# Kernel optimization log

Hardware: AMD Instinct MI355X
Metric: run time of the kernel (lower is better)

## Reference

```python
import jax, jax.numpy as jnp
import numpy as np

B, NQ, NK = 32, 1, 4096
Q_SIZE = K_SIZE = 512
H = 256


def setup_inputs() -> dict:
    key = jax.random.key(0)
    ks = jax.random.split(key, 6)
    return {
        "queries": jax.random.normal(ks[0], (B, NQ, Q_SIZE), jnp.float32),
        "keys": jax.random.normal(ks[1], (B, NK, K_SIZE), jnp.float32),
        "values": jax.random.normal(ks[2], (B, NK, 1), jnp.float32),
        "W_q": jax.random.normal(ks[3], (Q_SIZE, H), jnp.float32) / np.sqrt(Q_SIZE),
        "W_k": jax.random.normal(ks[4], (K_SIZE, H), jnp.float32) / np.sqrt(K_SIZE),
        "w_v": jax.random.normal(ks[5], (H,), jnp.float32) / np.sqrt(H),
    }


def reference(queries, keys, values, W_q, W_k, w_v):
    # Project queries and keys to hidden dim
    q = jnp.einsum("bqd,dh->bqh", queries, W_q)            # [B, NQ, H]
    k = jnp.einsum("bkd,dh->bkh", keys, W_k)               # [B, NK, H]
    # Broadcast-add + tanh: [B, NQ, NK, H]
    features = jnp.tanh(q[:, :, None, :] + k[:, None, :, :])
    # Reduce hidden dim with w_v -> scores [B, NQ, NK]
    scores = jnp.einsum("bqkh,h->bqk", features, w_v)
    attn = jax.nn.softmax(scores, axis=-1)                 # [B, NQ, NK]
    # Module squeezes n_q dim (==1) and trailing value dim (==1)
    return attn[:, 0, :] * values[:, :, 0]                 # [B, NK]
```

## Files before the change

kernel.cpp:

```cpp
#include <hip/hip_runtime.h>
#include <cstdint>
#include <cstddef>

#define NB 32
#define NKEYS 4096
#define DQ 512
#define HDIM 256

#define BM 64
#define BK 64

typedef __attribute__((ext_vector_type(8))) short bf16x8;
typedef __attribute__((ext_vector_type(4))) float f32x4;

typedef __attribute__((address_space(1))) const unsigned int g_u32;
typedef __attribute__((address_space(3))) unsigned int l_u32;

__device__ __forceinline__ unsigned short f2bf(float f) {
    union { float f; unsigned u; } v; v.f = f;
    unsigned r = v.u + 0x7FFFu + ((v.u >> 16) & 1u);
    return (unsigned short)(r >> 16);
}

__device__ __forceinline__ float tanh_fast(float x) {
    float e = __expf(2.0f * x);
    return 1.0f - 2.0f / (e + 1.0f);
}

__device__ __forceinline__ void gload_lds16(const void* g, void* l) {
    __builtin_amdgcn_global_load_lds((g_u32*)g, (l_u32*)l, 16, 0, 0);
}

__global__ void k_prep_wkT(const float* __restrict__ Wk, unsigned short* __restrict__ WkT) {
    __shared__ unsigned short t[64][65];
    const int tid = threadIdx.x;
    const int dt = (blockIdx.x >> 2) << 6;
    const int ht = (blockIdx.x & 3) << 6;
    #pragma unroll
    for (int i = 0; i < 16; ++i) {
        int idx = tid + i * 256;
        int d = idx >> 6, h = idx & 63;
        t[d][h] = f2bf(Wk[(size_t)(dt + d) * HDIM + ht + h]);
    }
    __syncthreads();
    #pragma unroll
    for (int i = 0; i < 16; ++i) {
        int idx = tid + i * 256;
        int h = idx >> 6, d = idx & 63;
        WkT[(size_t)(ht + h) * DQ + dt + d] = t[d][h];
    }
}

__global__ void k_qproj(const float* __restrict__ q, const float* __restrict__ Wq,
                        float* __restrict__ qp) {
    __shared__ float qrow[DQ];
    __shared__ float part[256];
    const int blk = blockIdx.x;
    const int b = blk >> 2, hq = blk & 3;
    const int tid = threadIdx.x;
    qrow[tid]       = q[b * DQ + tid];
    qrow[tid + 256] = q[b * DQ + tid + 256];
    __syncthreads();
    const int h = (hq << 6) + (tid & 63);
    const int d0 = (tid >> 6) << 7;
    float s = 0.f;
    #pragma unroll 4
    for (int d = d0; d < d0 + 128; ++d)
        s += qrow[d] * Wq[d * HDIM + h];
    part[tid] = s;
    __syncthreads();
    if (tid < 64)
        qp[b * HDIM + (hq << 6) + tid] =
            part[tid] + part[tid + 64] + part[tid + 128] + part[tid + 192];
}

__global__ __launch_bounds__(256, 2) void k_scores(
        const float* __restrict__ keys, const unsigned short* __restrict__ WkT,
        const float* __restrict__ qp, const float* __restrict__ wv,
        float* __restrict__ scores) {
    __shared__ __align__(16) unsigned short As[2][BM * BK];
    __shared__ __align__(16) unsigned short Bs[2][HDIM * BK];
    float* s_rows = reinterpret_cast<float*>(&As[0][0]);

    const int tid  = threadIdx.x;
    const int lane = tid & 63;
    const int wid  = tid >> 6;
    const int row0 = blockIdx.x * BM;
    const int b    = row0 >> 12;
    const int l15  = lane & 15;
    const int l4   = lane >> 4;

    const int ar  = tid >> 4;
    const int ac4 = tid & 15;
    const float* aptr[4];
    int awoff[4];
    #pragma unroll
    for (int i = 0; i < 4; ++i) {
        const int row = ar + i * 16;
        aptr[i]  = keys + (size_t)(row0 + row) * DQ + ac4 * 4;
        awoff[i] = row * 128 + (((ac4 >> 1) ^ (row & 7)) << 4) + (ac4 & 1) * 8;
    }
    const int bcol = wid * 64 + (lane >> 3);
    const int bsw  = (lane & 7) ^ ((lane >> 3) & 7);
    const unsigned short* bptr = WkT + (size_t)bcol * DQ + bsw * 8;

    const int r7 = l15 & 7;
    const int asl0 = (l4 ^ r7) << 4;
    const int asl1 = ((4 + l4) ^ r7) << 4;

    f32x4 acc[4][4];
    #pragma unroll
    for (int i = 0; i < 4; ++i)
        #pragma unroll
        for (int j = 0; j < 4; ++j)
            acc[i][j] = (f32x4){0.f, 0.f, 0.f, 0.f};

    float4 rA1[4], rA2[4];

    #pragma unroll
    for (int q = 0; q < 8; ++q)
        gload_lds16(bptr + q * (8 * DQ), &Bs[0][(wid * 64 + q * 8) * BK]);
    {
        float4 t0[4];
        #pragma unroll
        for (int i = 0; i < 4; ++i) t0[i] = *reinterpret_cast<const float4*>(aptr[i]);
        #pragma unroll
        for (int i = 0; i < 4; ++i) {
            ushort4 h4;
            h4.x = f2bf(t0[i].x); h4.y = f2bf(t0[i].y);
            h4.z = f2bf(t0[i].z); h4.w = f2bf(t0[i].w);
            *reinterpret_cast<ushort4*>(reinterpret_cast<char*>(&As[0][0]) + awoff[i]) = h4;
        }
    }
    asm volatile("s_waitcnt vmcnt(0)" ::: "memory");
    asm volatile("s_waitcnt lgkmcnt(0)" ::: "memory");
    __builtin_amdgcn_s_barrier();
    #pragma unroll
    for (int i = 0; i < 4; ++i)
        rA1[i] = *reinterpret_cast<const float4*>(aptr[i] + 1 * BK);

    #pragma unroll
    for (int kt = 0; kt < 8; ++kt) {
        const int cur = kt & 1, nxt = cur ^ 1;
        if (kt < 7) {
            #pragma unroll
            for (int q = 0; q < 8; ++q)
                gload_lds16(bptr + (kt + 1) * BK + q * (8 * DQ),
                            &Bs[nxt][(wid * 64 + q * 8) * BK]);
        }
        const char* Ab = reinterpret_cast<const char*>(&As[cur][0]);
        const char* Bb = reinterpret_cast<const char*>(&Bs[cur][0]);
        #pragma unroll
        for (int kk = 0; kk < 2; ++kk) {
            const int sl = kk ? asl1 : asl0;
            bf16x8 a[4], bb[4];
            #pragma unroll
            for (int i = 0; i < 4; ++i)
                a[i] = *reinterpret_cast<const bf16x8*>(Ab + (i * 16 + l15) * 128 + sl);
            #pragma unroll
            for (int j = 0; j < 4; ++j)
                bb[j] = *reinterpret_cast<const bf16x8*>(Bb + (wid * 64 + j * 16 + l15) * 128 + sl);
            __builtin_amdgcn_s_setprio(1);
            #pragma unroll
            for (int i = 0; i < 4; ++i)
                #pragma unroll
                for (int j = 0; j < 4; ++j)
                    acc[i][j] = __builtin_amdgcn_mfma_f32_16x16x32_bf16(
                        a[i], bb[j], acc[i][j], 0, 0, 0);
            __builtin_amdgcn_s_setprio(0);
        }
        if (kt < 7) {
            #pragma unroll
            for (int i = 0; i < 4; ++i) {
                const float4 v = (kt & 1) ? rA2[i] : rA1[i];
                ushort4 h4;
                h4.x = f2bf(v.x); h4.y = f2bf(v.y); h4.z = f2bf(v.z); h4.w = f2bf(v.w);
                *reinterpret_cast<ushort4*>(
                    reinterpret_cast<char*>(&As[nxt][0]) + awoff[i]) = h4;
            }
            if (kt < 6) {
                #pragma unroll
                for (int i = 0; i < 4; ++i) {
                    const float4 v = *reinterpret_cast<const float4*>(aptr[i] + (kt + 2) * BK);
                    if (kt & 1) rA1[i] = v; else rA2[i] = v;
                }
                asm volatile("s_waitcnt vmcnt(4)" ::: "memory");
            } else {
                asm volatile("s_waitcnt vmcnt(0)" ::: "memory");
            }
            asm volatile("s_waitcnt lgkmcnt(0)" ::: "memory");
            __builtin_amdgcn_s_barrier();
        }
    }

    if (tid < BM) s_rows[tid] = 0.f;
    __syncthreads();

    float qv[4], wvv[4];
    #pragma unroll
    for (int j = 0; j < 4; ++j) {
        int col = wid * 64 + j * 16 + l15;
        qv[j]  = qp[b * HDIM + col];
        wvv[j] = wv[col];
    }
    #pragma unroll
    for (int i = 0; i < 4; ++i) {
        #pragma unroll
        for (int r = 0; r < 4; ++r) {
            float p = 0.f;
            #pragma unroll
            for (int j = 0; j < 4; ++j) {
                float x = acc[i][j][r] + qv[j];
                p += tanh_fast(x) * wvv[j];
            }
            p += __shfl_xor(p, 1);
            p += __shfl_xor(p, 2);
            p += __shfl_xor(p, 4);
            p += __shfl_xor(p, 8);
            if (l15 == 0)
                atomicAdd(&s_rows[i * 16 + l4 * 4 + r], p);
        }
    }
    __syncthreads();
    if (tid < BM) scores[row0 + tid] = s_rows[tid];
}

__global__ void k_softmax(const float* __restrict__ scores, const float* __restrict__ values,
                          float* __restrict__ out) {
    __shared__ float red[32];
    const int b = blockIdx.x, tid = threadIdx.x;
    const float* s = scores + b * NKEYS;
    float v[4];
    float m = -1e30f;
    #pragma unroll
    for (int i = 0; i < 4; ++i) { v[i] = s[tid + i * 1024]; m = fmaxf(m, v[i]); }
    #pragma unroll
    for (int off = 1; off < 64; off <<= 1) m = fmaxf(m, __shfl_xor(m, off));
    const int w = tid >> 6;
    if ((tid & 63) == 0) red[w] = m;
    __syncthreads();
    m = red[0];
    #pragma unroll
    for (int i = 1; i < 16; ++i) m = fmaxf(m, red[i]);
    float sum = 0.f;
    #pragma unroll
    for (int i = 0; i < 4; ++i) { v[i] = __expf(v[i] - m); sum += v[i]; }
    #pragma unroll
    for (int off = 1; off < 64; off <<= 1) sum += __shfl_xor(sum, off);
    if ((tid & 63) == 0) red[16 + w] = sum;
    __syncthreads();
    sum = red[16];
    #pragma unroll
    for (int i = 1; i < 16; ++i) sum += red[16 + i];
    const float inv = 1.0f / sum;
    #pragma unroll
    for (int i = 0; i < 4; ++i) {
        int n = tid + i * 1024;
        out[b * NKEYS + n] = v[i] * inv * values[b * NKEYS + n];
    }
}

extern "C" void kernel_launch(void* const* d_in, const int* in_sizes, int n_in,
                              void* d_out, int out_size, void* d_ws, size_t ws_size,
                              hipStream_t stream) {
    const float* queries = (const float*)d_in[0];
    const float* keys    = (const float*)d_in[1];
    const float* values  = (const float*)d_in[2];
    const float* Wq      = (const float*)d_in[3];
    const float* Wk      = (const float*)d_in[4];
    const float* wv      = (const float*)d_in[5];
    float* out = (float*)d_out;

    char* ws = (char*)d_ws;
    float* scores        = (float*)ws;
    float* qp            = (float*)(ws + 131072 * 4);
    unsigned short* WkT  = (unsigned short*)(ws + 131072 * 4 + 8192 * 4);

    hipLaunchKernelGGL(k_prep_wkT, dim3(32),   dim3(256),  0, stream, Wk, WkT);
    hipLaunchKernelGGL(k_qproj,    dim3(128),  dim3(256),  0, stream, queries, Wq, qp);
    hipLaunchKernelGGL(k_scores,   dim3(NB * NKEYS / BM), dim3(256), 0, stream,
                       keys, WkT, qp, wv, scores);
    hipLaunchKernelGGL(k_softmax,  dim3(NB),   dim3(1024), 0, stream, scores, values, out);
}
```

Baseline: 398.9 us.

## Single-buffer the per-wave B tile in LDS and raise occupancy to three blocks

Drops the double buffer for the W_k tile in LDS. This is safe because each wave only reads and writes its own 64-row slice of B. The next tile's B loads are issued after the first half-K MFMAs' LDS reads finish, overlapping the second half of the MFMAs. The smaller LDS footprint lets launch bounds ask for 3 blocks per CU, meant to raise occupancy and hide latency. In exchange the B loads have less prefetch distance, the vmcnt waits are reordered, and register pressure under the higher occupancy bound may cause spills.

```diff
diff --git a/kernel.cpp b/kernel.cpp
--- a/kernel.cpp
+++ b/kernel.cpp
@@ -74,12 +74,12 @@
             part[tid] + part[tid + 64] + part[tid + 128] + part[tid + 192];
 }
 
-__global__ __launch_bounds__(256, 2) void k_scores(
+__global__ __launch_bounds__(256, 3) void k_scores(
         const float* __restrict__ keys, const unsigned short* __restrict__ WkT,
         const float* __restrict__ qp, const float* __restrict__ wv,
         float* __restrict__ scores) {
     __shared__ __align__(16) unsigned short As[2][BM * BK];
-    __shared__ __align__(16) unsigned short Bs[2][HDIM * BK];
+    __shared__ __align__(16) unsigned short Bs[HDIM * BK];
     float* s_rows = reinterpret_cast<float*>(&As[0][0]);
 
     const int tid  = threadIdx.x;
@@ -119,7 +119,7 @@
 
     #pragma unroll
     for (int q = 0; q < 8; ++q)
-        gload_lds16(bptr + q * (8 * DQ), &Bs[0][(wid * 64 + q * 8) * BK]);
+        gload_lds16(bptr + q * (8 * DQ), &Bs[(wid * 64 + q * 8) * BK]);
     {
         float4 t0[4];
         #pragma unroll
@@ -142,33 +142,58 @@
     #pragma unroll
     for (int kt = 0; kt < 8; ++kt) {
         const int cur = kt & 1, nxt = cur ^ 1;
+        if (kt == 7) asm volatile("s_waitcnt vmcnt(0)" ::: "memory");
+        else         asm volatile("s_waitcnt vmcnt(4)" ::: "memory");
+
+        const char* Ab = reinterpret_cast<const char*>(&As[cur][0]);
+        const char* Bb = reinterpret_cast<const char*>(&Bs[0]);
+
+        bf16x8 a0[4], b0[4];
+        #pragma unroll
+        for (int i = 0; i < 4; ++i)
+            a0[i] = *reinterpret_cast<const bf16x8*>(Ab + (i * 16 + l15) * 128 + asl0);
+        #pragma unroll
+        for (int j = 0; j < 4; ++j)
+            b0[j] = *reinterpret_cast<const bf16x8*>(Bb + (wid * 64 + j * 16 + l15) * 128 + asl0);
+        __builtin_amdgcn_s_setprio(1);
+        #pragma unroll
+        for (int i = 0; i < 4; ++i)
+            #pragma unroll
+            for (int j = 0; j < 4; ++j)
+                acc[i][j] = __builtin_amdgcn_mfma_f32_16x16x32_bf16(a0[i], b0[j], acc[i][j], 0, 0, 0);
+        __builtin_amdgcn_s_setprio(0);
+
+        bf16x8 a1[4], b1[4];
+        #pragma unroll
+        for (int i = 0; i < 4; ++i)
+            a1[i] = *reinterpret_cast<const bf16x8*>(Ab + (i * 16 + l15) * 128 + asl1);
+        #pragma unroll
+        for (int j = 0; j < 4; ++j)
+            b1[j] = *reinterpret_cast<const bf16x8*>(Bb + (wid * 64 + j * 16 + l15) * 128 + asl1);
+
+        asm volatile("s_waitcnt lgkmcnt(0)" ::: "memory");
         if (kt < 7) {
             #pragma unroll
             for (int q = 0; q < 8; ++q)
                 gload_lds16(bptr + (kt + 1) * BK + q * (8 * DQ),
-                            &Bs[nxt][(wid * 64 + q * 8) * BK]);
-        }
-        const char* Ab = reinterpret_cast<const char*>(&As[cur][0]);
-        const char* Bb = reinterpret_cast<const char*>(&Bs[cur][0]);
-        #pragma unroll
-        for (int kk = 0; kk < 2; ++kk) {
-            const int sl = kk ? asl1 : asl0;
-            bf16x8 a[4], bb[4];
-            #pragma unroll
-            for (int i = 0; i < 4; ++i)
-                a[i] = *reinterpret_cast<const bf16x8*>(Ab + (i * 16 + l15) * 128 + sl);
+                            &Bs[(wid * 64 + q * 8) * BK]);
+        }
+        if (kt < 6) {
+            #pragma unroll
+            for (int i = 0; i < 4; ++i) {
+                const float4 v = *reinterpret_cast<const float4*>(aptr[i] + (kt + 2) * BK);
+                if (kt & 1) rA1[i] = v; else rA2[i] = v;
+            }
+        }
+
+        __builtin_amdgcn_s_setprio(1);
+        #pragma unroll
+        for (int i = 0; i < 4; ++i)
             #pragma unroll
             for (int j = 0; j < 4; ++j)
-                bb[j] = *reinterpret_cast<const bf16x8*>(Bb + (wid * 64 + j * 16 + l15) * 128 + sl);
-            __builtin_amdgcn_s_setprio(1);
-            #pragma unroll
-            for (int i = 0; i < 4; ++i)
-                #pragma unroll
-                for (int j = 0; j < 4; ++j)
-                    acc[i][j] = __builtin_amdgcn_mfma_f32_16x16x32_bf16(
-                        a[i], bb[j], acc[i][j], 0, 0, 0);
-            __builtin_amdgcn_s_setprio(0);
-        }
+                acc[i][j] = __builtin_amdgcn_mfma_f32_16x16x32_bf16(a1[i], b1[j], acc[i][j], 0, 0, 0);
+        __builtin_amdgcn_s_setprio(0);
+
         if (kt < 7) {
             #pragma unroll
             for (int i = 0; i < 4; ++i) {
@@ -177,16 +202,6 @@
                 h4.x = f2bf(v.x); h4.y = f2bf(v.y); h4.z = f2bf(v.z); h4.w = f2bf(v.w);
                 *reinterpret_cast<ushort4*>(
                     reinterpret_cast<char*>(&As[nxt][0]) + awoff[i]) = h4;
-            }
-            if (kt < 6) {
-                #pragma unroll
-                for (int i = 0; i < 4; ++i) {
-                    const float4 v = *reinterpret_cast<const float4*>(aptr[i] + (kt + 2) * BK);
-                    if (kt & 1) rA1[i] = v; else rA2[i] = v;
-                }
-                asm volatile("s_waitcnt vmcnt(4)" ::: "memory");
-            } else {
-                asm volatile("s_waitcnt vmcnt(0)" ::: "memory");
             }
             asm volatile("s_waitcnt lgkmcnt(0)" ::: "memory");
             __builtin_amdgcn_s_barrier();
```

Measured after the change: 396.1 us. About the same (-0.7%).
